# Kernel optimization log

Hardware: AMD Instinct MI355X
Metric: run time of the kernel (lower is better)

Reference implementation:

```python
import jax, jax.numpy as jnp
import numpy as np

MAX_LEN = 64  # max segment length (lengths are (i%16+1)*4 <= 64)
NEG_INF = jnp.float32(-1e30)


def setup_inputs() -> dict:
    key = jax.random.key(0)
    k1, k2, k3 = jax.random.split(key, 3)
    B, EACH, H = 46, 32, 1024
    S = B * EACH  # 1472 segments
    lens = ((np.arange(S) % 16 + 1) * 4).astype(np.int32)  # ragged, sum = 50048
    N = int(lens.sum())
    offsets = np.concatenate([[0], np.cumsum(lens)[:-1]]).astype(np.int32)
    cls_embedding = jax.random.normal(k1, (N, H), dtype=jnp.float32)
    W = jax.random.normal(k2, (H, 1), dtype=jnp.float32) * 0.02
    b = jnp.zeros((1,), dtype=jnp.float32)
    length = jnp.asarray(lens.reshape(B, EACH))
    # exactly one positive per segment (at a random valid position)
    pos = jax.random.randint(k3, (S,), 0, 1 << 30) % jnp.asarray(lens)
    target = jnp.zeros((N,), dtype=jnp.int32).at[jnp.asarray(offsets) + pos].set(1)
    return {"cls_embedding": cls_embedding, "W": W, "b": b,
            "length": length, "target": target}


def _segmented_double_softmax_ce(logits, lens, tgt, each_length):
    # logits: [N], lens: [S], tgt: [N] 0/1 ints
    S = lens.shape[0]
    N = logits.shape[0]
    offsets = jnp.concatenate([jnp.zeros((1,), jnp.int32),
                               jnp.cumsum(lens)[:-1].astype(jnp.int32)])
    pos = jnp.arange(MAX_LEN, dtype=jnp.int32)
    idx = offsets[:, None] + pos[None, :]              # [S, MAX_LEN]
    valid = pos[None, :] < lens[:, None]               # [S, MAX_LEN]
    idx_c = jnp.minimum(idx, N - 1)
    seg_logits = logits[idx_c]                          # [S, MAX_LEN]
    seg_tgt = tgt[idx_c]                                # [S, MAX_LEN]
    # faithful to original: softmax over segment, then CrossEntropyLoss
    # (which applies log_softmax AGAIN) on the softmax output
    p = jax.nn.softmax(jnp.where(valid, seg_logits, NEG_INF), axis=-1)
    lse2 = jax.nn.logsumexp(jnp.where(valid, p, NEG_INF), axis=-1)  # [S]
    t_idx = jnp.argmax(jnp.where(valid, seg_tgt, -1), axis=-1)       # [S]
    p_t = jnp.take_along_axis(p, t_idx[:, None], axis=-1)[:, 0]
    loss_per = lse2 - p_t                                            # [S]
    # replicate the loop's skip conditions
    i = jnp.arange(S)
    next_len = jnp.concatenate([lens[1:], jnp.ones((1,), lens.dtype)])
    skip_next_zero = (i > 0) & (i + 1 < S) & (next_len == 0)
    tgt_sum = jnp.sum(jnp.where(valid, seg_tgt, 0), axis=-1)
    skip_no_pos = ((i + 1) % each_length == 0) & (tgt_sum <= 0)
    include = (lens > 0) & (~skip_next_zero) & (~skip_no_pos)
    cnt = jnp.sum(include).astype(jnp.float32)
    denom = jnp.where(cnt > 0, cnt, jnp.float32(1e-4))
    loss = jnp.sum(jnp.where(include, loss_per, 0.0)) / denom
    return loss


def reference(cls_embedding, W, b, length, target):
    # dropout is identity (inference); classifier -> per-row score
    logits = (cls_embedding @ W + b)[:, 0]   # [N]
    lens = length.reshape(-1).astype(jnp.int32)
    tgt = target.reshape(-1)
    each_length = length.shape[-1]
    loss = _segmented_double_softmax_ce(logits, lens, tgt, each_length)
    return logits, loss
```

## Files before the change

### kernel.cpp

```cpp
#include <hip/hip_runtime.h>


#define EACH_LEN 32

__device__ inline float wave_sum_f(float v) {
#pragma unroll
    for (int o = 32; o > 0; o >>= 1) v += __shfl_xor(v, o, 64);
    return v;
}
__device__ inline float wave_max_f(float v) {
#pragma unroll
    for (int o = 32; o > 0; o >>= 1) v = fmaxf(v, __shfl_xor(v, o, 64));
    return v;
}
__device__ inline int wave_sum_i(int v) {
#pragma unroll
    for (int o = 32; o > 0; o >>= 1) v += __shfl_xor(v, o, 64);
    return v;
}
__device__ inline int wave_max_i(int v) {
#pragma unroll
    for (int o = 32; o > 0; o >>= 1) v = max(v, __shfl_xor(v, o, 64));
    return v;
}

__global__ __launch_bounds__(256) void fused_kernel(
    const float* __restrict__ A, const float* __restrict__ W,
    const float* __restrict__ b, const int* __restrict__ lens,
    const int* __restrict__ tgt, float* __restrict__ logits,
    float* __restrict__ contrib, float* __restrict__ incl, int S) {
    const int tid = threadIdx.x, wid = tid >> 6, lane = tid & 63;

    int s0, s1;
    if ((S & 15) == 0) {
        const int g = blockIdx.x >> 3, j = blockIdx.x & 7;
        s0 = g * 16 + j;
        s1 = g * 16 + 15 - j;
    } else {
        s0 = blockIdx.x * 2;
        s1 = (s0 + 1 < S) ? s0 + 1 : -1;
    }

    const int hi = max(s0, s1);
    int p0 = 0, p1 = 0;
    for (int j = tid; j < hi; j += 256) {
        const int l = lens[j];
        if (j < s0) p0 += l;
        if (j < s1) p1 += l;
    }
    p0 = wave_sum_i(p0);
    p1 = wave_sum_i(p1);
    __shared__ int w0[4], w1[4];
    if (lane == 0) { w0[wid] = p0; w1[wid] = p1; }
    __syncthreads();
    const int off0 = w0[0] + w0[1] + w0[2] + w0[3];
    const int off1 = w1[0] + w1[1] + w1[2] + w1[3];
    const int len0 = lens[s0];
    const int len1 = (s1 >= 0) ? lens[s1] : 0;

    const float4* w4 = reinterpret_cast<const float4*>(W);
    const float4 wv0 = w4[lane], wv1 = w4[lane + 64],
                 wv2 = w4[lane + 128], wv3 = w4[lane + 192];
    const float bias = b[0];

    __shared__ float slog[128];
    const int R = len0 + len1;
    for (int r = wid; r < R; r += 4) {
        const int row = (r < len0) ? (off0 + r) : (off1 + (r - len0));
        const float4* a4 = reinterpret_cast<const float4*>(A + (size_t)row * 1024);
        float acc = 0.f;
        float4 av;
        av = a4[lane];
        acc = fmaf(av.x, wv0.x, acc); acc = fmaf(av.y, wv0.y, acc);
        acc = fmaf(av.z, wv0.z, acc); acc = fmaf(av.w, wv0.w, acc);
        av = a4[lane + 64];
        acc = fmaf(av.x, wv1.x, acc); acc = fmaf(av.y, wv1.y, acc);
        acc = fmaf(av.z, wv1.z, acc); acc = fmaf(av.w, wv1.w, acc);
        av = a4[lane + 128];
        acc = fmaf(av.x, wv2.x, acc); acc = fmaf(av.y, wv2.y, acc);
        acc = fmaf(av.z, wv2.z, acc); acc = fmaf(av.w, wv2.w, acc);
        av = a4[lane + 192];
        acc = fmaf(av.x, wv3.x, acc); acc = fmaf(av.y, wv3.y, acc);
        acc = fmaf(av.z, wv3.z, acc); acc = fmaf(av.w, wv3.w, acc);
        acc = wave_sum_f(acc);
        if (lane == 0) {
            const float v = acc + bias;
            slog[r] = v;
            logits[row] = v;
        }
    }
    __syncthreads();

    if (wid < 2) {
        const int s = wid ? s1 : s0;
        if (s >= 0) {
            const int len  = wid ? len1 : len0;
            const int off  = wid ? off1 : off0;
            const int base = wid ? len0 : 0;
            const bool valid = lane < len;

            const float l = valid ? slog[base + lane] : -3.402823e38f;
            const float m = wave_max_f(l);
            const float e = valid ? __expf(l - m) : 0.f;
            const float Z = wave_sum_f(e);
            const float p = e / Z;

            const float q = valid ? __expf(p) : 0.f;
            const float lse2 = __logf(wave_sum_f(q));

            const int tv = valid ? tgt[off + lane] : -1;
            const int maxt = wave_max_i(tv);
            const unsigned long long ball = __ballot(tv == maxt);
            const int t_idx = __ffsll(ball) - 1;
            const float p_t = __shfl(p, t_idx, 64);

            const int tgt_sum = wave_sum_i(valid ? tv : 0);

            const int next_len = (s + 1 < S) ? lens[s + 1] : 1;
            const bool skip_next_zero = (s > 0) && (s + 1 < S) && (next_len == 0);
            const bool skip_no_pos = (((s + 1) % EACH_LEN) == 0) && (tgt_sum <= 0);
            const bool include = (len > 0) && !skip_next_zero && !skip_no_pos;

            if (lane == 0) {
                contrib[s] = include ? (lse2 - p_t) : 0.f;
                incl[s]    = include ? 1.f : 0.f;
            }
        }
    }
}

__global__ __launch_bounds__(256) void reduce_kernel(
    const float* __restrict__ contrib, const float* __restrict__ incl,
    float* __restrict__ out_loss, int S) {
    float a = 0.f, c = 0.f;
    for (int i = threadIdx.x; i < S; i += 256) {
        a += contrib[i];
        c += incl[i];
    }
    a = wave_sum_f(a);
    c = wave_sum_f(c);
    __shared__ float wa[4], wc[4];
    const int wid = threadIdx.x >> 6, lane = threadIdx.x & 63;
    if (lane == 0) { wa[wid] = a; wc[wid] = c; }
    __syncthreads();
    if (threadIdx.x == 0) {
        const float A = wa[0] + wa[1] + wa[2] + wa[3];
        const float C = wc[0] + wc[1] + wc[2] + wc[3];
        const float denom = (C > 0.f) ? C : 1e-4f;
        out_loss[0] = A / denom;
    }
}

extern "C" void kernel_launch(void* const* d_in, const int* in_sizes, int n_in,
                              void* d_out, int out_size, void* d_ws, size_t ws_size,
                              hipStream_t stream) {
    const float* A   = (const float*)d_in[0];
    const float* W   = (const float*)d_in[1];
    const float* b   = (const float*)d_in[2];
    const int*  lens = (const int*)d_in[3];
    const int*  tgt  = (const int*)d_in[4];

    const int H = in_sizes[1];
    const int N = in_sizes[0] / H;
    const int S = in_sizes[3];

    float* logits = (float*)d_out;
    float* loss   = logits + N;

    float* contrib = (float*)d_ws;
    float* incl    = contrib + S;

    const int nblk = (S + 1) / 2;
    fused_kernel<<<nblk, 256, 0, stream>>>(A, W, b, lens, tgt,
                                           logits, contrib, incl, S);
    reduce_kernel<<<1, 256, 0, stream>>>(contrib, incl, loss, S);
}
```

Measured before the change: 39.15 us.

## Fuse final loss reduction via atomics and process two rows per wave

Replaces the separate single-block reduction kernel with atomic accumulation plus a last-block-done counter, so the loss finishes inside the main kernel, with a small memset added to zero the accumulator. Each wave now computes two row dot products at once, giving more loads in flight. Logit stores are also coalesced through shared memory. The exchange is a memset launch, contended atomics and a non-deterministic float summation order.

```diff
diff --git a/kernel.cpp b/kernel.cpp
--- a/kernel.cpp
+++ b/kernel.cpp
@@ -28,7 +28,8 @@
     const float* __restrict__ A, const float* __restrict__ W,
     const float* __restrict__ b, const int* __restrict__ lens,
     const int* __restrict__ tgt, float* __restrict__ logits,
-    float* __restrict__ contrib, float* __restrict__ incl, int S) {
+    float* __restrict__ acc_sum, unsigned* __restrict__ counter,
+    float* __restrict__ loss, int S) {
     const int tid = threadIdx.x, wid = tid >> 6, lane = tid & 63;
 
     int s0, s1;
@@ -59,37 +60,45 @@
     const int len1 = (s1 >= 0) ? lens[s1] : 0;
 
     const float4* w4 = reinterpret_cast<const float4*>(W);
-    const float4 wv0 = w4[lane], wv1 = w4[lane + 64],
-                 wv2 = w4[lane + 128], wv3 = w4[lane + 192];
+    float4 wv[4];
+    wv[0] = w4[lane];       wv[1] = w4[lane + 64];
+    wv[2] = w4[lane + 128]; wv[3] = w4[lane + 192];
     const float bias = b[0];
 
     __shared__ float slog[128];
     const int R = len0 + len1;
-    for (int r = wid; r < R; r += 4) {
-        const int row = (r < len0) ? (off0 + r) : (off1 + (r - len0));
-        const float4* a4 = reinterpret_cast<const float4*>(A + (size_t)row * 1024);
-        float acc = 0.f;
-        float4 av;
-        av = a4[lane];
-        acc = fmaf(av.x, wv0.x, acc); acc = fmaf(av.y, wv0.y, acc);
-        acc = fmaf(av.z, wv0.z, acc); acc = fmaf(av.w, wv0.w, acc);
-        av = a4[lane + 64];
-        acc = fmaf(av.x, wv1.x, acc); acc = fmaf(av.y, wv1.y, acc);
-        acc = fmaf(av.z, wv1.z, acc); acc = fmaf(av.w, wv1.w, acc);
-        av = a4[lane + 128];
-        acc = fmaf(av.x, wv2.x, acc); acc = fmaf(av.y, wv2.y, acc);
-        acc = fmaf(av.z, wv2.z, acc); acc = fmaf(av.w, wv2.w, acc);
-        av = a4[lane + 192];
-        acc = fmaf(av.x, wv3.x, acc); acc = fmaf(av.y, wv3.y, acc);
-        acc = fmaf(av.z, wv3.z, acc); acc = fmaf(av.w, wv3.w, acc);
-        acc = wave_sum_f(acc);
+    for (int r0 = wid * 2; r0 < R; r0 += 8) {
+        const int rA = r0, rB = r0 + 1;
+        const bool hasB = rB < R;
+        const int rowA = (rA < len0) ? (off0 + rA) : (off1 + (rA - len0));
+        const int rBc  = hasB ? rB : rA;
+        const int rowB = (rBc < len0) ? (off0 + rBc) : (off1 + (rBc - len0));
+        const float4* a4A = reinterpret_cast<const float4*>(A + (size_t)rowA * 1024);
+        const float4* a4B = reinterpret_cast<const float4*>(A + (size_t)rowB * 1024);
+        float accA = 0.f, accB = 0.f;
+#pragma unroll
+        for (int k = 0; k < 4; ++k) {
+            const float4 avA = a4A[lane + 64 * k];
+            const float4 avB = a4B[lane + 64 * k];
+            accA = fmaf(avA.x, wv[k].x, accA); accA = fmaf(avA.y, wv[k].y, accA);
+            accA = fmaf(avA.z, wv[k].z, accA); accA = fmaf(avA.w, wv[k].w, accA);
+            accB = fmaf(avB.x, wv[k].x, accB); accB = fmaf(avB.y, wv[k].y, accB);
+            accB = fmaf(avB.z, wv[k].z, accB); accB = fmaf(avB.w, wv[k].w, accB);
+        }
+#pragma unroll
+        for (int o = 32; o > 0; o >>= 1) {
+            accA += __shfl_xor(accA, o, 64);
+            accB += __shfl_xor(accB, o, 64);
+        }
         if (lane == 0) {
-            const float v = acc + bias;
-            slog[r] = v;
-            logits[row] = v;
+            slog[rA] = accA + bias;
+            if (hasB) slog[rB] = accB + bias;
         }
     }
     __syncthreads();
+
+    if (tid < len0) logits[off0 + tid] = slog[tid];
+    if (tid < len1) logits[off1 + tid] = slog[len0 + tid];
 
     if (wid < 2) {
         const int s = wid ? s1 : s0;
@@ -121,33 +130,22 @@
             const bool skip_no_pos = (((s + 1) % EACH_LEN) == 0) && (tgt_sum <= 0);
             const bool include = (len > 0) && !skip_next_zero && !skip_no_pos;
 
-            if (lane == 0) {
-                contrib[s] = include ? (lse2 - p_t) : 0.f;
-                incl[s]    = include ? 1.f : 0.f;
+            if (lane == 0 && include) {
+                atomicAdd(&acc_sum[0], lse2 - p_t);
+                atomicAdd(&acc_sum[1], 1.f);
             }
         }
     }
-}
+    __syncthreads();
 
-__global__ __launch_bounds__(256) void reduce_kernel(
-    const float* __restrict__ contrib, const float* __restrict__ incl,
-    float* __restrict__ out_loss, int S) {
-    float a = 0.f, c = 0.f;
-    for (int i = threadIdx.x; i < S; i += 256) {
-        a += contrib[i];
-        c += incl[i];
-    }
-    a = wave_sum_f(a);
-    c = wave_sum_f(c);
-    __shared__ float wa[4], wc[4];
-    const int wid = threadIdx.x >> 6, lane = threadIdx.x & 63;
-    if (lane == 0) { wa[wid] = a; wc[wid] = c; }
-    __syncthreads();
-    if (threadIdx.x == 0) {
-        const float A = wa[0] + wa[1] + wa[2] + wa[3];
-        const float C = wc[0] + wc[1] + wc[2] + wc[3];
-        const float denom = (C > 0.f) ? C : 1e-4f;
-        out_loss[0] = A / denom;
+    if (tid == 0) {
+        __threadfence();
+        const unsigned old = atomicAdd(counter, 1u);
+        if (old == gridDim.x - 1) {
+            const float Asum = atomicAdd(&acc_sum[0], 0.f);
+            const float Csum = atomicAdd(&acc_sum[1], 0.f);
+            loss[0] = Asum / (Csum > 0.f ? Csum : 1e-4f);
+        }
     }
 }
 
@@ -167,11 +165,12 @@
     float* logits = (float*)d_out;
     float* loss   = logits + N;
 
-    float* contrib = (float*)d_ws;
-    float* incl    = contrib + S;
+    float*    acc     = (float*)d_ws;
+    unsigned* counter = (unsigned*)d_ws + 2;
+
+    hipMemsetAsync(d_ws, 0, 12, stream);
 
     const int nblk = (S + 1) / 2;
     fused_kernel<<<nblk, 256, 0, stream>>>(A, W, b, lens, tgt,
-                                           logits, contrib, incl, S);
-    reduce_kernel<<<1, 256, 0, stream>>>(contrib, incl, loss, S);
+                                           logits, acc, counter, loss, S);
 }
```

New measurement: 84.12 us. +114.9%, slower.
